# Kernel optimization log

Measured on AMD Instinct MI355X. Metric: run time of the kernel, lower is better.

The kernel has to match this reference:

```python
import jax, jax.numpy as jnp
import numpy as np

D_MODEL = 1024
NUM_HEADS = 16
D_K = D_MODEL // NUM_HEADS


def setup_inputs() -> dict:
    key = jax.random.key(0)
    k1, k2, k3 = jax.random.split(key, 3)
    x = jax.random.normal(k1, (2, 2048, D_MODEL), dtype=jnp.float32)
    # torch Linear(d, 3d): weight shape [3d, d], y = x @ W.T
    W_QKV = jax.random.normal(k2, (3 * D_MODEL, D_MODEL), dtype=jnp.float32) * (1.0 / np.sqrt(D_MODEL))
    W_O = jax.random.normal(k3, (D_MODEL, D_MODEL), dtype=jnp.float32) * (1.0 / np.sqrt(D_MODEL))
    return {"x": x, "W_QKV": W_QKV, "W_O": W_O}


def reference(x, W_QKV, W_O):
    B, T, C = x.shape
    qkv = jnp.einsum('btc,fc->btf', x, W_QKV)  # [B,T,3C]
    q, k, v = jnp.split(qkv, 3, axis=-1)
    def heads(t):
        return t.reshape(B, T, NUM_HEADS, D_K).transpose(0, 2, 1, 3)  # [B,H,T,Dk]
    Q, K, V = heads(q), heads(k), heads(v)
    scores = jnp.einsum('bhqd,bhkd->bhqk', Q, K) / jnp.sqrt(jnp.float32(D_K))
    causal = jnp.tril(jnp.ones((T, T), dtype=bool))
    scores = jnp.where(causal, scores, -jnp.inf)
    attn = jax.nn.softmax(scores, axis=-1)
    out = jnp.einsum('bhqk,bhkd->bhqd', attn, V)
    out = out.transpose(0, 2, 1, 3).reshape(B, T, C)
    return jnp.einsum('btc,oc->bto', out, W_O)
```

## Files before the change

kernel.cpp:

```cpp
#include <hip/hip_runtime.h>
#include <hip/hip_bf16.h>
#include <stdint.h>
#include <stddef.h>


typedef __attribute__((ext_vector_type(8)))  __bf16   bf16x8;
typedef __attribute__((ext_vector_type(4)))  float    f32x4;
typedef __attribute__((ext_vector_type(16))) float    f32x16;
typedef __attribute__((ext_vector_type(4)))  uint32_t u32x4;

#define AS1(p) ((__attribute__((address_space(1))) void*)(p))
#define AS3(p) ((__attribute__((address_space(3))) void*)(p))

static constexpr int Tq    = 2048;
static constexpr int Cd    = 1024;
static constexpr int Mrows = 2 * Tq;

#define QSCALE 0.18033688011112042f

__global__ __launch_bounds__(256) void cvt_bf16_kernel(const float* __restrict__ in,
                                                       __bf16* __restrict__ out, int n8)
{
    int idx    = blockIdx.x * blockDim.x + threadIdx.x;
    int stride = gridDim.x * blockDim.x;
    for (int i = idx; i < n8; i += stride) {
        f32x4 a = ((const f32x4*)in)[i * 2 + 0];
        f32x4 b = ((const f32x4*)in)[i * 2 + 1];
        bf16x8 o;
#pragma unroll
        for (int j = 0; j < 4; ++j) { o[j] = (__bf16)a[j]; o[4 + j] = (__bf16)b[j]; }
        ((bf16x8*)out)[i] = o;
    }
}

__global__ __launch_bounds__(256) void transpose_v_kernel(const __bf16* __restrict__ qkv,
                                                          __bf16* __restrict__ vT)
{
    __shared__ __bf16 tile[64][65];
    const int t   = threadIdx.x;
    const int r0  = blockIdx.x * 64;
    const int hd0 = blockIdx.y * 64;

    {
        const int rr = t >> 2, c16 = (t & 3) * 16;
        const __bf16* src = qkv + (size_t)(r0 + rr) * 3072 + 2048 + hd0 + c16;
        bf16x8 a = *(const bf16x8*)(src);
        bf16x8 b = *(const bf16x8*)(src + 8);
#pragma unroll
        for (int j = 0; j < 8; ++j) { tile[rr][c16 + j] = a[j]; tile[rr][c16 + 8 + j] = b[j]; }
    }
    __syncthreads();
    {
        const int hd_loc = t >> 2, rg = (t & 3) * 16;
        bf16x8 a, b;
#pragma unroll
        for (int j = 0; j < 8; ++j) { a[j] = tile[rg + j][hd_loc]; b[j] = tile[rg + 8 + j][hd_loc]; }
        __bf16* dst = vT + (size_t)(hd0 + hd_loc) * Mrows + r0 + rg;
        *(bf16x8*)(dst)     = a;
        *(bf16x8*)(dst + 8) = b;
    }
}

template <bool OUT_BF16>
__global__ __launch_bounds__(256) void gemm_bt_kernel(const __bf16* __restrict__ A,
                                                      const __bf16* __restrict__ Bm,
                                                      float* __restrict__ Cf,
                                                      __bf16* __restrict__ Cb,
                                                      int N, int K, int qcols, float qscale)
{
    __shared__ __align__(16) __bf16 As[128 * 64];
    __shared__ __align__(16) __bf16 Bs[128 * 64];

    const int tid = threadIdx.x;
    const int l   = tid & 63;
    const int w   = tid >> 6;
    const int wr  = w >> 1, wc = w & 1;
    const int lo  = l & 15, hi = l >> 4;
    const int m0  = blockIdx.x * 128;
    const int n0  = blockIdx.y * 128;

    f32x4 acc[4][4] = {};

    for (int kk = 0; kk < K; kk += 64) {
#pragma unroll
        for (int i = 0; i < 4; ++i) {
            int s   = i * 256 + tid;
            int row = s >> 3;
            int gg  = (s & 7) ^ (row & 7);
            const __bf16* srcA = A  + (size_t)(m0 + row) * K + kk + gg * 8;
            const __bf16* srcB = Bm + (size_t)(n0 + row) * K + kk + gg * 8;
            __builtin_amdgcn_global_load_lds(AS1(srcA), AS3((char*)As + s * 16), 16, 0, 0);
            __builtin_amdgcn_global_load_lds(AS1(srcB), AS3((char*)Bs + s * 16), 16, 0, 0);
        }
        __syncthreads();

#pragma unroll
        for (int ks = 0; ks < 2; ++ks) {
            bf16x8 af[4], bfr[4];
#pragma unroll
            for (int m = 0; m < 4; ++m) {
                int row = wr * 64 + m * 16 + lo;
                int gl  = (ks * 4 + hi) ^ (row & 7);
                af[m] = *(const bf16x8*)((const char*)As + row * 128 + gl * 16);
            }
#pragma unroll
            for (int n = 0; n < 4; ++n) {
                int row = wc * 64 + n * 16 + lo;
                int gl  = (ks * 4 + hi) ^ (row & 7);
                bfr[n] = *(const bf16x8*)((const char*)Bs + row * 128 + gl * 16);
            }
#pragma unroll
            for (int m = 0; m < 4; ++m)
#pragma unroll
                for (int n = 0; n < 4; ++n)
                    acc[m][n] = __builtin_amdgcn_mfma_f32_16x16x32_bf16(af[m], bfr[n], acc[m][n], 0, 0, 0);
        }
        __syncthreads();
    }

#pragma unroll
    for (int m = 0; m < 4; ++m)
#pragma unroll
        for (int n = 0; n < 4; ++n)
#pragma unroll
            for (int r = 0; r < 4; ++r) {
                int row = m0 + wr * 64 + m * 16 + hi * 4 + r;
                int col = n0 + wc * 64 + n * 16 + lo;
                float v = acc[m][n][r];
                if (col < qcols) v *= qscale;
                if (OUT_BF16) Cb[(size_t)row * N + col] = (__bf16)v;
                else          Cf[(size_t)row * N + col] = v;
            }
}

__global__ __launch_bounds__(128) void attn_chunk_kernel(const __bf16* __restrict__ qkv,
                                                         const __bf16* __restrict__ vT,
                                                         __bf16* __restrict__ att,
                                                         float* __restrict__ pO,
                                                         float* __restrict__ stats)
{
    constexpr uint8_t QT[48] = {16,17,18,19,20,21,22,23,24,25,26,27,28,29,30,31,
                                15,31,14,30,13,29,12,28,11,27,10,26, 9,25, 8,24,
                                 7,23, 6,22, 5,21, 4,20, 3,19, 2,18, 1,17, 0,16};
    constexpr uint8_t CC[48] = {0,0,0,0,0,0,0,0,0,0,0,0,0,0,0,0,
                                255,1,255,1,255,1,255,1,255,1,255,1,255,1,255,1,
                                255,1,255,1,255,1,255,1,255,1,255,1,255,1,255,1};

    __shared__ __align__(16) __bf16 Ks[2][64 * 64];
    __shared__ __align__(16) __bf16 Vs[2][64 * 64];

    const int tid = threadIdx.x;
    const int l   = tid & 63;
    const int w   = tid >> 6;
    const int lo5 = l & 31, hi5 = l >> 5;

    const int bid = blockIdx.x;
    const int ord = bid >> 5;
    const int bh  = bid & 31;
    const int h   = bh & 15;
    const int b   = bh >> 4;

    const int  qt     = QT[ord];
    const int  cc     = CC[ord];
    const bool direct = (cc == 255);
    const int  t0     = direct ? 0 : cc * 16;
    const int  t1     = direct ? qt + 1 : min(cc * 16 + 16, qt + 1);
    const int  qb0    = qt * 64;

    const __bf16* Kbase = qkv + (size_t)b * Tq * 3072 + 1024 + h * 64;
    const __bf16* Vbase = vT  + (size_t)h * 64 * Mrows + b * Tq;

    bf16x8 onesf;
#pragma unroll
    for (int jj = 0; jj < 8; ++jj) onesf[jj] = (__bf16)1.0f;

    bf16x8 qf[4];
    {
        const __bf16* Qp = qkv + (size_t)(b * Tq + qb0 + w * 32 + lo5) * 3072 + h * 64 + hi5 * 8;
#pragma unroll
        for (int ds = 0; ds < 4; ++ds) qf[ds] = *(const bf16x8*)(Qp + ds * 16);
    }

    f32x16 o0 = {}, o1 = {}, ls = {};
    float m = -1e30f;

#pragma unroll
    for (int i = 0; i < 4; ++i) {
        int s = i * 128 + tid;
        int row = s >> 3, gg = (s & 7) ^ (row & 7);
        __builtin_amdgcn_global_load_lds(AS1(Kbase + (size_t)(t0 * 64 + row) * 3072 + gg * 8),
                                         AS3((char*)Ks[0] + s * 16), 16, 0, 0);
        __builtin_amdgcn_global_load_lds(AS1(Vbase + (size_t)row * Mrows + t0 * 64 + gg * 8),
                                         AS3((char*)Vs[0] + s * 16), 16, 0, 0);
    }
    __syncthreads();

    int cur = 0;
    for (int t = t0; t < t1; ++t) {
        if (t + 1 < t1) {
            const int kn = (t + 1) * 64;
#pragma unroll
            for (int i = 0; i < 4; ++i) {
                int s = i * 128 + tid;
                int row = s >> 3, gg = (s & 7) ^ (row & 7);
                __builtin_amdgcn_global_load_lds(AS1(Kbase + (size_t)(kn + row) * 3072 + gg * 8),
                                                 AS3((char*)Ks[cur ^ 1] + s * 16), 16, 0, 0);
                __builtin_amdgcn_global_load_lds(AS1(Vbase + (size_t)row * Mrows + kn + gg * 8),
                                                 AS3((char*)Vs[cur ^ 1] + s * 16), 16, 0, 0);
            }
        }

        f32x16 sf0 = {}, sf1 = {};
        __builtin_amdgcn_s_setprio(1);
#pragma unroll
        for (int ds = 0; ds < 4; ++ds) {
            {
                int row = lo5;
                int gl  = (ds * 2 + hi5) ^ (row & 7);
                bf16x8 kf = *(const bf16x8*)((const char*)Ks[cur] + row * 128 + gl * 16);
                sf0 = __builtin_amdgcn_mfma_f32_32x32x16_bf16(kf, qf[ds], sf0, 0, 0, 0);
            }
            {
                int row = 32 + lo5;
                int gl  = (ds * 2 + hi5) ^ (row & 7);
                bf16x8 kf = *(const bf16x8*)((const char*)Ks[cur] + row * 128 + gl * 16);
                sf1 = __builtin_amdgcn_mfma_f32_32x32x16_bf16(kf, qf[ds], sf1, 0, 0, 0);
            }
        }
        __builtin_amdgcn_s_setprio(0);

        if (t == qt) {
            const int ql = w * 32 + lo5;
#pragma unroll
            for (int r = 0; r < 16; ++r) {
                int kc = (r & 3) + 8 * (r >> 2) + 4 * hi5;
                if (kc      > ql) sf0[r] = -1e30f;
                if (kc + 32 > ql) sf1[r] = -1e30f;
            }
        }

        float t0m = fmaxf(sf0[0],  fmaxf(sf0[1],  sf0[2]));
        float t1m = fmaxf(sf0[3],  fmaxf(sf0[4],  sf0[5]));
        float t2m = fmaxf(sf0[6],  fmaxf(sf0[7],  sf0[8]));
        float t3m = fmaxf(sf0[9],  fmaxf(sf0[10], sf0[11]));
        float t4m = fmaxf(sf0[12], fmaxf(sf0[13], sf0[14]));
        float t5m = fmaxf(sf1[0],  fmaxf(sf1[1],  sf1[2]));
        float t6m = fmaxf(sf1[3],  fmaxf(sf1[4],  sf1[5]));
        float t7m = fmaxf(sf1[6],  fmaxf(sf1[7],  sf1[8]));
        float t8m = fmaxf(sf1[9],  fmaxf(sf1[10], sf1[11]));
        float t9m = fmaxf(sf1[12], fmaxf(sf1[13], sf1[14]));
        float u0 = fmaxf(t0m, fmaxf(t1m, t2m));
        float u1 = fmaxf(t3m, fmaxf(t4m, sf0[15]));
        float u2 = fmaxf(t5m, fmaxf(t6m, t7m));
        float u3 = fmaxf(t8m, fmaxf(t9m, sf1[15]));
        float pmh = fmaxf(fmaxf(u0, u1), fmaxf(u2, u3));
        float pm  = fmaxf(pmh, __shfl_xor(pmh, 32));

        if (__any(pm > m + 8.0f)) {
            float mnew = fmaxf(m, pm);
            float fac  = __builtin_amdgcn_exp2f(m - mnew);
            m = mnew;
#pragma unroll
            for (int r = 0; r < 16; ++r) {
                int qreg = (r & 3) + 8 * (r >> 2) + 4 * hi5;
                float fr = __shfl(fac, qreg);
                o0[r] *= fr;
                o1[r] *= fr;
                ls[r] *= fr;
            }
        }

        __builtin_amdgcn_s_setprio(1);
#pragma unroll
        for (int kb = 0; kb < 2; ++kb) {
            uint32_t W[8];
#pragma unroll
            for (int wd = 0; wd < 8; ++wd) {
                float sa = (kb == 0) ? sf0[2 * wd]     : sf1[2 * wd];
                float sb = (kb == 0) ? sf0[2 * wd + 1] : sf1[2 * wd + 1];
                __bf16 ba = (__bf16)__builtin_amdgcn_exp2f(sa - m);
                __bf16 bb = (__bf16)__builtin_amdgcn_exp2f(sb - m);
                W[wd] = (uint32_t)__builtin_bit_cast(uint16_t, ba)
                      | ((uint32_t)__builtin_bit_cast(uint16_t, bb) << 16);
            }
            uint32_t Za = __shfl_xor(hi5 ? W[0] : W[2], 32);
            uint32_t Zb = __shfl_xor(hi5 ? W[1] : W[3], 32);
            uint32_t Zc = __shfl_xor(hi5 ? W[4] : W[6], 32);
            uint32_t Zd = __shfl_xor(hi5 ? W[5] : W[7], 32);

            {
                u32x4 fw = { hi5 ? Za : W[0], hi5 ? Zb : W[1],
                             hi5 ? W[2] : Za, hi5 ? W[3] : Zb };
                bf16x8 pa = __builtin_bit_cast(bf16x8, fw);
                const int kstep = kb * 2;
                {
                    int row = lo5;
                    int gl  = (kstep * 2 + hi5) ^ (row & 7);
                    bf16x8 vb = *(const bf16x8*)((const char*)Vs[cur] + row * 128 + gl * 16);
                    o0 = __builtin_amdgcn_mfma_f32_32x32x16_bf16(pa, vb, o0, 0, 0, 0);
                }
                {
                    int row = 32 + lo5;
                    int gl  = (kstep * 2 + hi5) ^ (row & 7);
                    bf16x8 vb = *(const bf16x8*)((const char*)Vs[cur] + row * 128 + gl * 16);
                    o1 = __builtin_amdgcn_mfma_f32_32x32x16_bf16(pa, vb, o1, 0, 0, 0);
                }
                ls = __builtin_amdgcn_mfma_f32_32x32x16_bf16(pa, onesf, ls, 0, 0, 0);
            }
            {
                u32x4 fw = { hi5 ? Zc : W[4], hi5 ? Zd : W[5],
                             hi5 ? W[6] : Zc, hi5 ? W[7] : Zd };
                bf16x8 pa = __builtin_bit_cast(bf16x8, fw);
                const int kstep = kb * 2 + 1;
                {
                    int row = lo5;
                    int gl  = (kstep * 2 + hi5) ^ (row & 7);
                    bf16x8 vb = *(const bf16x8*)((const char*)Vs[cur] + row * 128 + gl * 16);
                    o0 = __builtin_amdgcn_mfma_f32_32x32x16_bf16(pa, vb, o0, 0, 0, 0);
                }
                {
                    int row = 32 + lo5;
                    int gl  = (kstep * 2 + hi5) ^ (row & 7);
                    bf16x8 vb = *(const bf16x8*)((const char*)Vs[cur] + row * 128 + gl * 16);
                    o1 = __builtin_amdgcn_mfma_f32_32x32x16_bf16(pa, vb, o1, 0, 0, 0);
                }
                ls = __builtin_amdgcn_mfma_f32_32x32x16_bf16(pa, onesf, ls, 0, 0, 0);
            }
        }
        __builtin_amdgcn_s_setprio(0);

        __syncthreads();
        cur ^= 1;
    }

    if (direct) {
#pragma unroll
        for (int r = 0; r < 16; ++r) {
            float lr   = __builtin_amdgcn_rcpf(ls[r]);
            int   qreg = (r & 3) + 8 * (r >> 2) + 4 * hi5;
            int   rowg = b * Tq + qb0 + w * 32 + qreg;
            att[(size_t)rowg * Cd + h * 64 + lo5]      = (__bf16)(o0[r] * lr);
            att[(size_t)rowg * Cd + h * 64 + 32 + lo5] = (__bf16)(o1[r] * lr);
        }
    } else {
        const int slot = bh * 32 + (qt - 16) * 2 + cc;
        float* po = pO + (size_t)slot * 4096;
#pragma unroll
        for (int r = 0; r < 16; ++r) {
            int   qreg = (r & 3) + 8 * (r >> 2) + 4 * hi5;
            int   row  = w * 32 + qreg;
            po[row * 64 + lo5]      = o0[r];
            po[row * 64 + 32 + lo5] = o1[r];
            float mq = __shfl(m, qreg);
            if (lo5 == 0) {
                stats[(size_t)slot * 128 + row * 2 + 0] = mq;
                stats[(size_t)slot * 128 + row * 2 + 1] = ls[r];
            }
        }
    }
}

__global__ __launch_bounds__(256) void attn_merge_kernel(const float* __restrict__ pO,
                                                         const float* __restrict__ stats,
                                                         __bf16* __restrict__ att)
{
    const int mo  = blockIdx.x;
    const int bh  = mo & 31;
    const int qq  = mo >> 5;
    const int qt  = 16 + qq;
    const int h   = bh & 15;
    const int b   = bh >> 4;

    const int slot0 = bh * 32 + qq * 2;
    const int slot1 = slot0 + 1;

    const int tid = threadIdx.x;
    const int row = tid >> 2;
    const int c16 = (tid & 3) * 16;

    float m0 = stats[(size_t)slot0 * 128 + row * 2 + 0];
    float l0 = stats[(size_t)slot0 * 128 + row * 2 + 1];
    float m1 = stats[(size_t)slot1 * 128 + row * 2 + 0];
    float l1 = stats[(size_t)slot1 * 128 + row * 2 + 1];
    float M  = fmaxf(m0, m1);
    float w0 = exp2f(m0 - M);
    float w1 = exp2f(m1 - M);
    float inv = 1.0f / (w0 * l0 + w1 * l1);

    const float* p0 = pO + (size_t)slot0 * 4096 + row * 64 + c16;
    const float* p1 = pO + (size_t)slot1 * 4096 + row * 64 + c16;

    bf16x8 ov[2];
#pragma unroll
    for (int i = 0; i < 4; ++i) {
        f32x4 a = ((const f32x4*)p0)[i];
        f32x4 bb = ((const f32x4*)p1)[i];
#pragma unroll
        for (int j = 0; j < 4; ++j)
            ov[i >> 1][(i & 1) * 4 + j] = (__bf16)((w0 * a[j] + w1 * bb[j]) * inv);
    }
    __bf16* dst = att + (size_t)(b * Tq + qt * 64 + row) * Cd + h * 64 + c16;
    *(bf16x8*)(dst)     = ov[0];
    *(bf16x8*)(dst + 8) = ov[1];
}

extern "C" void kernel_launch(void* const* d_in, const int* in_sizes, int n_in,
                              void* d_out, int out_size, void* d_ws, size_t ws_size,
                              hipStream_t stream)
{
    (void)in_sizes; (void)n_in; (void)out_size; (void)ws_size;

    const float* x    = (const float*)d_in[0];
    const float* Wqkv = (const float*)d_in[1];
    const float* Wo   = (const float*)d_in[2];
    float*       out  = (float*)d_out;

    char* ws = (char*)d_ws;
    __bf16* xb    = (__bf16*)(ws);
    __bf16* wqkvb = (__bf16*)(ws + (size_t)8  * 1024 * 1024);
    __bf16* wob   = (__bf16*)(ws + (size_t)14 * 1024 * 1024);
    __bf16* qkvb  = (__bf16*)(ws + (size_t)16 * 1024 * 1024);
    __bf16* attb  = (__bf16*)(ws + (size_t)40 * 1024 * 1024);
    __bf16* vTb   = xb;
    float*  stats = (float*)wqkvb;
    float*  pO    = out;

    cvt_bf16_kernel<<<2048, 256, 0, stream>>>(x,    xb,    Mrows * Cd / 8);
    cvt_bf16_kernel<<<1536, 256, 0, stream>>>(Wqkv, wqkvb, 3 * Cd * Cd / 8);
    cvt_bf16_kernel<<<512,  256, 0, stream>>>(Wo,   wob,   Cd * Cd / 8);

    dim3 g1(Mrows / 128, 3 * Cd / 128);
    gemm_bt_kernel<true><<<g1, 256, 0, stream>>>(xb, wqkvb, nullptr, qkvb, 3 * Cd, Cd,
                                                 1024, QSCALE);

    dim3 gt(Mrows / 64, Cd / 64);
    transpose_v_kernel<<<gt, 256, 0, stream>>>(qkvb, vTb);

    attn_chunk_kernel<<<1536, 128, 0, stream>>>(qkvb, vTb, attb, pO, stats);
    attn_merge_kernel<<<512, 256, 0, stream>>>(pO, stats, attb);

    dim3 g2(Mrows / 128, Cd / 128);
    gemm_bt_kernel<false><<<g2, 256, 0, stream>>>(attb, wob, out, nullptr, Cd, Cd,
                                                  0, 1.0f);
}
```

Measured before the change: 208.6 us.

## Double attention query tile to 128 rows with four waves per block

The attention kernel now processes 128 query rows per block with 256 threads (four waves) instead of 64 rows with two waves. Each K/V tile loaded into shared memory is therefore reused by twice as many queries, which halves K/V global traffic and block count. The causal mask is generalized to per-wave global positions, and the split/merge schedule tables, slot sizes and merge kernel are adjusted to match. The cost is fewer blocks (768), coarser load balance, and wasted masked work on diagonal tiles.

```diff
diff --git a/kernel.cpp b/kernel.cpp
--- a/kernel.cpp
+++ b/kernel.cpp
@@ -133,18 +133,18 @@
             }
 }
 
-__global__ __launch_bounds__(128) void attn_chunk_kernel(const __bf16* __restrict__ qkv,
+__global__ __launch_bounds__(256) void attn_chunk_kernel(const __bf16* __restrict__ qkv,
                                                          const __bf16* __restrict__ vT,
                                                          __bf16* __restrict__ att,
                                                          float* __restrict__ pO,
                                                          float* __restrict__ stats)
 {
-    constexpr uint8_t QT[48] = {16,17,18,19,20,21,22,23,24,25,26,27,28,29,30,31,
-                                15,31,14,30,13,29,12,28,11,27,10,26, 9,25, 8,24,
-                                 7,23, 6,22, 5,21, 4,20, 3,19, 2,18, 1,17, 0,16};
-    constexpr uint8_t CC[48] = {0,0,0,0,0,0,0,0,0,0,0,0,0,0,0,0,
-                                255,1,255,1,255,1,255,1,255,1,255,1,255,1,255,1,
-                                255,1,255,1,255,1,255,1,255,1,255,1,255,1,255,1};
+    constexpr uint8_t QT[24] = { 8, 9,10,11,12,13,14,15,
+                                15, 7,14, 6,13, 5,12, 4,
+                                11, 3,10, 2, 9, 1, 8, 0};
+    constexpr uint8_t CC[24] = { 0, 0, 0, 0, 0, 0, 0, 0,
+                                 1,255, 1,255, 1,255, 1,255,
+                                 1,255, 1,255, 1,255, 1,255};
 
     __shared__ __align__(16) __bf16 Ks[2][64 * 64];
     __shared__ __align__(16) __bf16 Vs[2][64 * 64];
@@ -163,9 +163,10 @@
     const int  qt     = QT[ord];
     const int  cc     = CC[ord];
     const bool direct = (cc == 255);
+    const int  ntall  = 2 * qt + 2;
     const int  t0     = direct ? 0 : cc * 16;
-    const int  t1     = direct ? qt + 1 : min(cc * 16 + 16, qt + 1);
-    const int  qb0    = qt * 64;
+    const int  t1     = direct ? ntall : min(cc * 16 + 16, ntall);
+    const int  qb0    = qt * 128;
 
     const __bf16* Kbase = qkv + (size_t)b * Tq * 3072 + 1024 + h * 64;
     const __bf16* Vbase = vT  + (size_t)h * 64 * Mrows + b * Tq;
@@ -174,9 +175,11 @@
 #pragma unroll
     for (int jj = 0; jj < 8; ++jj) onesf[jj] = (__bf16)1.0f;
 
+    const int qg = qb0 + w * 32 + lo5;
+
     bf16x8 qf[4];
     {
-        const __bf16* Qp = qkv + (size_t)(b * Tq + qb0 + w * 32 + lo5) * 3072 + h * 64 + hi5 * 8;
+        const __bf16* Qp = qkv + (size_t)(b * Tq + qg) * 3072 + h * 64 + hi5 * 8;
 #pragma unroll
         for (int ds = 0; ds < 4; ++ds) qf[ds] = *(const bf16x8*)(Qp + ds * 16);
     }
@@ -185,8 +188,8 @@
     float m = -1e30f;
 
 #pragma unroll
-    for (int i = 0; i < 4; ++i) {
-        int s = i * 128 + tid;
+    for (int i = 0; i < 2; ++i) {
+        int s = i * 256 + tid;
         int row = s >> 3, gg = (s & 7) ^ (row & 7);
         __builtin_amdgcn_global_load_lds(AS1(Kbase + (size_t)(t0 * 64 + row) * 3072 + gg * 8),
                                          AS3((char*)Ks[0] + s * 16), 16, 0, 0);
@@ -200,8 +203,8 @@
         if (t + 1 < t1) {
             const int kn = (t + 1) * 64;
 #pragma unroll
-            for (int i = 0; i < 4; ++i) {
-                int s = i * 128 + tid;
+            for (int i = 0; i < 2; ++i) {
+                int s = i * 256 + tid;
                 int row = s >> 3, gg = (s & 7) ^ (row & 7);
                 __builtin_amdgcn_global_load_lds(AS1(Kbase + (size_t)(kn + row) * 3072 + gg * 8),
                                                  AS3((char*)Ks[cur ^ 1] + s * 16), 16, 0, 0);
@@ -229,13 +232,12 @@
         }
         __builtin_amdgcn_s_setprio(0);
 
-        if (t == qt) {
-            const int ql = w * 32 + lo5;
+        if (t * 64 + 63 > qb0 + w * 32) {
 #pragma unroll
             for (int r = 0; r < 16; ++r) {
-                int kc = (r & 3) + 8 * (r >> 2) + 4 * hi5;
-                if (kc      > ql) sf0[r] = -1e30f;
-                if (kc + 32 > ql) sf1[r] = -1e30f;
+                int kcg = t * 64 + (r & 3) + 8 * (r >> 2) + 4 * hi5;
+                if (kcg      > qg) sf0[r] = -1e30f;
+                if (kcg + 32 > qg) sf1[r] = -1e30f;
             }
         }
 
@@ -343,8 +345,8 @@
             att[(size_t)rowg * Cd + h * 64 + 32 + lo5] = (__bf16)(o1[r] * lr);
         }
     } else {
-        const int slot = bh * 32 + (qt - 16) * 2 + cc;
-        float* po = pO + (size_t)slot * 4096;
+        const int slot = bh * 16 + (qt - 8) * 2 + cc;
+        float* po = pO + (size_t)slot * 8192;
 #pragma unroll
         for (int r = 0; r < 16; ++r) {
             int   qreg = (r & 3) + 8 * (r >> 2) + 4 * hi5;
@@ -353,8 +355,8 @@
             po[row * 64 + 32 + lo5] = o1[r];
             float mq = __shfl(m, qreg);
             if (lo5 == 0) {
-                stats[(size_t)slot * 128 + row * 2 + 0] = mq;
-                stats[(size_t)slot * 128 + row * 2 + 1] = ls[r];
+                stats[(size_t)slot * 256 + row * 2 + 0] = mq;
+                stats[(size_t)slot * 256 + row * 2 + 1] = ls[r];
             }
         }
     }
@@ -367,41 +369,41 @@
     const int mo  = blockIdx.x;
     const int bh  = mo & 31;
     const int qq  = mo >> 5;
-    const int qt  = 16 + qq;
+    const int qt  = 8 + qq;
     const int h   = bh & 15;
     const int b   = bh >> 4;
 
-    const int slot0 = bh * 32 + qq * 2;
+    const int slot0 = bh * 16 + qq * 2;
     const int slot1 = slot0 + 1;
 
     const int tid = threadIdx.x;
-    const int row = tid >> 2;
-    const int c16 = (tid & 3) * 16;
-
-    float m0 = stats[(size_t)slot0 * 128 + row * 2 + 0];
-    float l0 = stats[(size_t)slot0 * 128 + row * 2 + 1];
-    float m1 = stats[(size_t)slot1 * 128 + row * 2 + 0];
-    float l1 = stats[(size_t)slot1 * 128 + row * 2 + 1];
+    const int row = tid >> 1;
+    const int c0  = (tid & 1) * 32;
+
+    float m0 = stats[(size_t)slot0 * 256 + row * 2 + 0];
+    float l0 = stats[(size_t)slot0 * 256 + row * 2 + 1];
+    float m1 = stats[(size_t)slot1 * 256 + row * 2 + 0];
+    float l1 = stats[(size_t)slot1 * 256 + row * 2 + 1];
     float M  = fmaxf(m0, m1);
     float w0 = exp2f(m0 - M);
     float w1 = exp2f(m1 - M);
     float inv = 1.0f / (w0 * l0 + w1 * l1);
 
-    const float* p0 = pO + (size_t)slot0 * 4096 + row * 64 + c16;
-    const float* p1 = pO + (size_t)slot1 * 4096 + row * 64 + c16;
-
-    bf16x8 ov[2];
-#pragma unroll
-    for (int i = 0; i < 4; ++i) {
-        f32x4 a = ((const f32x4*)p0)[i];
+    const float* p0 = pO + (size_t)slot0 * 8192 + row * 64 + c0;
+    const float* p1 = pO + (size_t)slot1 * 8192 + row * 64 + c0;
+
+    bf16x8 ov[4];
+#pragma unroll
+    for (int i = 0; i < 8; ++i) {
+        f32x4 a  = ((const f32x4*)p0)[i];
         f32x4 bb = ((const f32x4*)p1)[i];
 #pragma unroll
         for (int j = 0; j < 4; ++j)
             ov[i >> 1][(i & 1) * 4 + j] = (__bf16)((w0 * a[j] + w1 * bb[j]) * inv);
     }
-    __bf16* dst = att + (size_t)(b * Tq + qt * 64 + row) * Cd + h * 64 + c16;
-    *(bf16x8*)(dst)     = ov[0];
-    *(bf16x8*)(dst + 8) = ov[1];
+    __bf16* dst = att + (size_t)(b * Tq + qt * 128 + row) * Cd + h * 64 + c0;
+#pragma unroll
+    for (int i = 0; i < 4; ++i) *(bf16x8*)(dst + i * 8) = ov[i];
 }
 
 extern "C" void kernel_launch(void* const* d_in, const int* in_sizes, int n_in,
@@ -436,8 +438,8 @@
     dim3 gt(Mrows / 64, Cd / 64);
     transpose_v_kernel<<<gt, 256, 0, stream>>>(qkvb, vTb);
 
-    attn_chunk_kernel<<<1536, 128, 0, stream>>>(qkvb, vTb, attb, pO, stats);
-    attn_merge_kernel<<<512, 256, 0, stream>>>(pO, stats, attb);
+    attn_chunk_kernel<<<768, 256, 0, stream>>>(qkvb, vTb, attb, pO, stats);
+    attn_merge_kernel<<<256, 256, 0, stream>>>(pO, stats, attb);
 
     dim3 g2(Mrows / 128, Cd / 128);
     gemm_bt_kernel<false><<<g2, 256, 0, stream>>>(attb, wob, out, nullptr, Cd, Cd,
```

Result: faster. 193.0 us (-7.5%).
